# Kernel optimization log

Hardware: AMD Instinct MI355X
Metric: run time of the kernel (lower is better)

## Reference

```python
import jax, jax.numpy as jnp
import numpy as np

S, B, V, E, H = 512, 256, 100000, 128, 256


def setup_inputs() -> dict:
    key = jax.random.key(0)
    k1, k2, k3, k4, k5, k6 = jax.random.split(key, 6)
    X = jax.random.randint(k1, (S, B), 0, V)
    emb = jax.random.normal(k2, (V, E), dtype=jnp.float32)
    # PyTorch nn.RNN init: U(-1/sqrt(H), 1/sqrt(H))
    s = 1.0 / np.sqrt(H)
    W_ih = jax.random.uniform(k3, (H, E), minval=-s, maxval=s, dtype=jnp.float32)
    W_hh = jax.random.uniform(k4, (H, H), minval=-s, maxval=s, dtype=jnp.float32)
    b_ih = jax.random.uniform(k5, (H,), minval=-s, maxval=s, dtype=jnp.float32)
    b_hh = jax.random.uniform(k6, (H,), minval=-s, maxval=s, dtype=jnp.float32)
    return {"X": X, "emb": emb, "W_ih": W_ih, "W_hh": W_hh, "b_ih": b_ih, "b_hh": b_hh}


def reference(X, emb, W_ih, W_hh, b_ih, b_hh):
    embedded = emb[X]                                   # [S, B, E]
    # Precompute input projections for all timesteps (one big GEMM)
    xproj = jnp.einsum('sbe,he->sbh', embedded, W_ih) + b_ih + b_hh  # [S, B, H]
    h0 = jnp.zeros((B, H), dtype=embedded.dtype)

    def step(h, xp):
        h_new = jnp.tanh(xp + h @ W_hh.T)
        return h_new, None

    h_last, _ = jax.lax.scan(step, h0, xproj)           # [B, H]
    return jax.nn.log_softmax(h_last, axis=1)
```

## Files before the change

kernel.cpp:

```cpp
#include <hip/hip_runtime.h>
#include <math.h>

#define S_LEN 512
#define B_SZ  256
#define E_SZ  128
#define H_SZ  256
#define XSTP  65536

typedef __attribute__((ext_vector_type(8))) short bf16x8;
typedef __attribute__((ext_vector_type(4))) float f32x4;

__device__ short g_wfh[H_SZ * E_SZ];
__device__ short g_wfl[H_SZ * E_SZ];

__device__ __forceinline__ unsigned pkbf(float a, float b) {
    unsigned r; asm("v_cvt_pk_bf16_f32 %0, %1, %2" : "=v"(r) : "v"(a), "v"(b));
    return r;
}
__device__ __forceinline__ float fromlo(unsigned u) {
    union { unsigned u; float f; } c; c.u = u << 16; return c.f;
}
__device__ __forceinline__ float fromhi(unsigned u) {
    union { unsigned u; float f; } c; c.u = u & 0xffff0000u; return c.f;
}
__device__ __forceinline__ void cvt_hilo8(float4 a, float4 b, bf16x8& hi, bf16x8& lo) {
    unsigned h0 = pkbf(a.x, a.y), h1 = pkbf(a.z, a.w);
    unsigned h2 = pkbf(b.x, b.y), h3 = pkbf(b.z, b.w);
    unsigned l0 = pkbf(a.x - fromlo(h0), a.y - fromhi(h0));
    unsigned l1 = pkbf(a.z - fromlo(h1), a.w - fromhi(h1));
    unsigned l2 = pkbf(b.x - fromlo(h2), b.y - fromhi(h2));
    unsigned l3 = pkbf(b.z - fromlo(h3), b.w - fromhi(h3));
    union { bf16x8 v; unsigned u[4]; } H, L;
    H.u[0] = h0; H.u[1] = h1; H.u[2] = h2; H.u[3] = h3;
    L.u[0] = l0; L.u[1] = l1; L.u[2] = l2; L.u[3] = l3;
    hi = H.v; lo = L.v;
}

__device__ __forceinline__ float tanhC(float v) {
    float e = __builtin_amdgcn_exp2f(v * 2.8853900818f);
    return fmaf(-2.f, __builtin_amdgcn_rcpf(e + 1.f), 1.f);
}

__global__ void prep_w_kernel(const float* __restrict__ W_ih) {
    const int t  = blockIdx.x * 256 + threadIdx.x;
    const int l  = t & 63;
    const int kk = (t >> 6) & 3;
    const int ht = t >> 8;
    const int h  = ht * 16 + (l & 15);
    const int k0 = kk * 32 + (l >> 4) * 8;
    const float* wp = W_ih + h * E_SZ + k0;
    float4 a = *(const float4*)wp;
    float4 b = *(const float4*)(wp + 4);
    bf16x8 hi, lo;
    cvt_hilo8(a, b, hi, lo);
    *(bf16x8*)&g_wfh[t * 8] = hi;
    *(bf16x8*)&g_wfl[t * 8] = lo;
}

__global__ __launch_bounds__(256) void embed_proj_mfma(
    const int*   __restrict__ X,
    const float* __restrict__ emb,
    const float* __restrict__ b_ih,
    const float* __restrict__ b_hh,
    float*       __restrict__ xproj)
{
    __shared__ int   toks[32];
    __shared__ short BtH[2][4][64][8];
    __shared__ short BtL[2][4][64][8];

    const int tid  = threadIdx.x;
    const int wave = tid >> 6;
    const int lane = tid & 63;
    const int quad = lane >> 4;
    const size_t row0 = (size_t)blockIdx.x * 32;
    const int s_idx = (int)(row0 >> 8);
    const int bbase = (int)(row0 & 255);

    if (tid < 32) toks[tid] = X[row0 + tid];
    __syncthreads();

    {
        const int r  = tid >> 3;
        const int kk = (tid >> 1) & 3;
        const int hq = tid & 1;
        const float* ep = emb + (size_t)toks[r] * E_SZ + kk * 32 + hq * 16;
        float4 a0 = ((const float4*)ep)[0];
        float4 b0 = ((const float4*)ep)[1];
        float4 a1 = ((const float4*)ep)[2];
        float4 b1 = ((const float4*)ep)[3];
        bf16x8 h0, l0, h1, l1;
        cvt_hilo8(a0, b0, h0, l0);
        cvt_hilo8(a1, b1, h1, l1);
        const int q0 = hq * 2, rl = r & 15, nt = r >> 4;
        *(bf16x8*)&BtH[nt][kk][q0 * 16 + rl][0]       = h0;
        *(bf16x8*)&BtL[nt][kk][q0 * 16 + rl][0]       = l0;
        *(bf16x8*)&BtH[nt][kk][(q0 + 1) * 16 + rl][0] = h1;
        *(bf16x8*)&BtL[nt][kk][(q0 + 1) * 16 + rl][0] = l1;
    }
    __syncthreads();

#pragma unroll
    for (int mt = 0; mt < 4; ++mt) {
        const int ht = wave * 4 + mt;
        bf16x8 wh[4], wl[4];
#pragma unroll
        for (int kk = 0; kk < 4; ++kk) {
            wh[kk] = *(const bf16x8*)&g_wfh[((ht * 4 + kk) * 64 + lane) * 8];
            wl[kk] = *(const bf16x8*)&g_wfl[((ht * 4 + kk) * 64 + lane) * 8];
        }

        f32x4 acc0 = {0.f, 0.f, 0.f, 0.f};
        f32x4 acc1 = {0.f, 0.f, 0.f, 0.f};
#pragma unroll
        for (int kk = 0; kk < 4; ++kk) {
            bf16x8 bh0  = *(const bf16x8*)&BtH[0][kk][lane][0];
            bf16x8 blo0 = *(const bf16x8*)&BtL[0][kk][lane][0];
            bf16x8 bh1  = *(const bf16x8*)&BtH[1][kk][lane][0];
            bf16x8 blo1 = *(const bf16x8*)&BtL[1][kk][lane][0];
            acc0 = __builtin_amdgcn_mfma_f32_16x16x32_bf16(wh[kk], bh0,  acc0, 0, 0, 0);
            acc0 = __builtin_amdgcn_mfma_f32_16x16x32_bf16(wh[kk], blo0, acc0, 0, 0, 0);
            acc0 = __builtin_amdgcn_mfma_f32_16x16x32_bf16(wl[kk], bh0,  acc0, 0, 0, 0);
            acc1 = __builtin_amdgcn_mfma_f32_16x16x32_bf16(wh[kk], bh1,  acc1, 0, 0, 0);
            acc1 = __builtin_amdgcn_mfma_f32_16x16x32_bf16(wh[kk], blo1, acc1, 0, 0, 0);
            acc1 = __builtin_amdgcn_mfma_f32_16x16x32_bf16(wl[kk], bh1,  acc1, 0, 0, 0);
        }

        const int hb = ht * 16 + quad * 4;
        float4 bi  = *(const float4*)&b_ih[hb];
        float4 bh4 = *(const float4*)&b_hh[hb];
#pragma unroll
        for (int nt = 0; nt < 2; ++nt) {
            const int b   = bbase + nt * 16;
            const int blk = b >> 5, str = (b >> 4) & 1;
            f32x4 o = (nt == 0) ? acc0 : acc1;
            o[0] += bi.x + bh4.x; o[1] += bi.y + bh4.y;
            o[2] += bi.z + bh4.z; o[3] += bi.w + bh4.w;
            float* dst = xproj + (size_t)s_idx * XSTP
                       + ((((blk * 2 + str) * 8 + (ht >> 1)) * 2 + (ht & 1)) * 64 + lane) * 4;
            *(f32x4*)dst = o;
        }
    }
}

__global__ __launch_bounds__(512) void rnn_scan_kernel(
    const float* __restrict__ xproj,
    const float* __restrict__ W_hh,
    float*       __restrict__ out)
{
    const int tid  = threadIdx.x;
    const int wave = tid >> 6;
    const int lane = tid & 63;
    const int bl   = lane & 15;
    const int quad = lane >> 4;
    const int B0   = blockIdx.x * 16;

    __shared__ short HB[2][4096];
    __shared__ float sred[8][16];

    bf16x8 wfrag[2][8];
#pragma unroll
    for (int mt = 0; mt < 2; ++mt) {
        const int h = wave * 32 + mt * 16 + bl;
#pragma unroll
        for (int kk = 0; kk < 8; ++kk) {
            const float* wp = W_hh + (size_t)h * H_SZ + kk * 32 + quad * 8;
            float4 a = *(const float4*)wp;
            float4 b = *(const float4*)(wp + 4);
            union { bf16x8 v; unsigned u[4]; } F;
            F.u[0] = pkbf(a.x, a.y); F.u[1] = pkbf(a.z, a.w);
            F.u[2] = pkbf(b.x, b.y); F.u[3] = pkbf(b.z, b.w);
            wfrag[mt][kk] = F.v;
        }
    }

    ((int4*)&HB[0][0])[tid] = make_int4(0, 0, 0, 0);

    const int xsw = (bl & 8) << 2;

    const short* rd0 = &HB[0][0] + ((lane * 8) ^ xsw);
    const short* rd1 = &HB[1][0] + ((lane * 8) ^ xsw);

    const int wo = (wave * 512 + (quad >> 1) * 128 + bl * 8 + (quad & 1) * 4) ^ xsw;
    short* const w0 = &HB[0][0] + wo;
    short* const w1 = &HB[1][0] + wo;

    const float* xpb = xproj + ((size_t)blockIdx.x * 16 + wave * 2) * 256 + lane * 4;

    f32x4 xe0 = *(const f32x4*)(xpb);
    f32x4 xe1 = *(const f32x4*)(xpb + 256);
    f32x4 xo0 = *(const f32x4*)(xpb + XSTP);
    f32x4 xo1 = *(const f32x4*)(xpb + XSTP + 256);

    __syncthreads();

    auto do_step = [&](const short* rd, short* wr,
                       f32x4& x0, f32x4& x1, const float* pf) {
        bf16x8 bf[8];
#pragma unroll
        for (int kk = 0; kk < 8; ++kk)
            bf[kk] = *(const bf16x8*)(rd + kk * 512);

        f32x4 a0 = x0, b0 = {0.f,0.f,0.f,0.f};
#pragma unroll
        for (int kk = 0; kk < 4; ++kk) {
            a0 = __builtin_amdgcn_mfma_f32_16x16x32_bf16(wfrag[0][kk],   bf[kk],   a0, 0, 0, 0);
            b0 = __builtin_amdgcn_mfma_f32_16x16x32_bf16(wfrag[0][kk+4], bf[kk+4], b0, 0, 0, 0);
        }
        f32x4 a1 = x1, b1 = {0.f,0.f,0.f,0.f};
#pragma unroll
        for (int kk = 0; kk < 4; ++kk) {
            a1 = __builtin_amdgcn_mfma_f32_16x16x32_bf16(wfrag[1][kk],   bf[kk],   a1, 0, 0, 0);
            b1 = __builtin_amdgcn_mfma_f32_16x16x32_bf16(wfrag[1][kk+4], bf[kk+4], b1, 0, 0, 0);
        }

        const f32x4 d0 = a0 + b0;
        float t0 = tanhC(d0[0]), t1 = tanhC(d0[1]), t2 = tanhC(d0[2]), t3 = tanhC(d0[3]);
        *(uint2*)wr = make_uint2(pkbf(t0, t1), pkbf(t2, t3));

        const f32x4 d1 = a1 + b1;
        float u0 = tanhC(d1[0]), u1 = tanhC(d1[1]), u2 = tanhC(d1[2]), u3 = tanhC(d1[3]);
        *(uint2*)(wr + 256) = make_uint2(pkbf(u0, u1), pkbf(u2, u3));

        x0 = *(const f32x4*)pf;
        x1 = *(const f32x4*)(pf + 256);

        asm volatile("s_waitcnt lgkmcnt(0)" ::: "memory");
        __builtin_amdgcn_sched_barrier(0);
        __builtin_amdgcn_s_barrier();
    };

    const float* pf = xpb + 2 * (size_t)XSTP;
    for (int s = 0; s < 510; s += 2) {
        do_step(rd0, w1, xe0, xe1, pf);
        do_step(rd1, w0, xo0, xo1, pf + XSTP);
        pf += 2 * (size_t)XSTP;
    }
    do_step(rd0, w1, xe0, xe1, xpb);

    float vf0[4], vf1[4];
    {
        bf16x8 bf[8];
#pragma unroll
        for (int kk = 0; kk < 8; ++kk)
            bf[kk] = *(const bf16x8*)(rd1 + kk * 512);
        f32x4 a0 = xo0, a1 = xo1;
        f32x4 b0 = {0.f,0.f,0.f,0.f}, b1 = {0.f,0.f,0.f,0.f};
#pragma unroll
        for (int kk = 0; kk < 4; ++kk) {
            a0 = __builtin_amdgcn_mfma_f32_16x16x32_bf16(wfrag[0][kk],   bf[kk],   a0, 0, 0, 0);
            a1 = __builtin_amdgcn_mfma_f32_16x16x32_bf16(wfrag[1][kk],   bf[kk],   a1, 0, 0, 0);
            b0 = __builtin_amdgcn_mfma_f32_16x16x32_bf16(wfrag[0][kk+4], bf[kk+4], b0, 0, 0, 0);
            b1 = __builtin_amdgcn_mfma_f32_16x16x32_bf16(wfrag[1][kk+4], bf[kk+4], b1, 0, 0, 0);
        }
        const f32x4 d0 = a0 + b0, d1 = a1 + b1;
#pragma unroll
        for (int r = 0; r < 4; ++r) {
            vf0[r] = tanhC(d0[r]);
            vf1[r] = tanhC(d1[r]);
        }
    }

    float m = fmaxf(fmaxf(fmaxf(vf0[0], vf0[1]), fmaxf(vf0[2], vf0[3])),
                    fmaxf(fmaxf(vf1[0], vf1[1]), fmaxf(vf1[2], vf1[3])));
    m = fmaxf(m, __shfl_xor(m, 16));
    m = fmaxf(m, __shfl_xor(m, 32));
    if (lane < 16) sred[wave][bl] = m;
    __syncthreads();
    float mall = sred[0][bl];
#pragma unroll
    for (int w = 1; w < 8; ++w) mall = fmaxf(mall, sred[w][bl]);
    __syncthreads();

    float ss = 0.f;
#pragma unroll
    for (int r = 0; r < 4; ++r)
        ss += __expf(vf0[r] - mall) + __expf(vf1[r] - mall);
    ss += __shfl_xor(ss, 16);
    ss += __shfl_xor(ss, 32);
    if (lane < 16) sred[wave][bl] = ss;
    __syncthreads();
    float tot = sred[0][bl];
#pragma unroll
    for (int w = 1; w < 8; ++w) tot += sred[w][bl];
    const float lse = mall + __logf(tot);

    f32x4 o0, o1;
#pragma unroll
    for (int r = 0; r < 4; ++r) { o0[r] = vf0[r] - lse; o1[r] = vf1[r] - lse; }
    float* op = out + (size_t)(B0 + bl) * H_SZ + wave * 32 + quad * 4;
    *(f32x4*)op        = o0;
    *(f32x4*)(op + 16) = o1;
}

extern "C" void kernel_launch(void* const* d_in, const int* in_sizes, int n_in,
                              void* d_out, int out_size, void* d_ws, size_t ws_size,
                              hipStream_t stream) {
    const int*   X    = (const int*)  d_in[0];
    const float* emb  = (const float*)d_in[1];
    const float* W_ih = (const float*)d_in[2];
    const float* W_hh = (const float*)d_in[3];
    const float* b_ih = (const float*)d_in[4];
    const float* b_hh = (const float*)d_in[5];
    float* out   = (float*)d_out;
    float* xproj = (float*)d_ws;

    prep_w_kernel<<<dim3(16), 256, 0, stream>>>(W_ih);
    embed_proj_mfma<<<dim3((S_LEN * B_SZ) / 32), 256, 0, stream>>>(
        X, emb, b_ih, b_hh, xproj);
    rnn_scan_kernel<<<dim3(B_SZ / 16), 512, 0, stream>>>(xproj, W_hh, out);
}
```

Baseline: 408.8 us.

## Fuse embedding projection and RNN scan into one kernel with per-timestep flags

Merges the embed/projection kernel and the recurrent scan into a single launch. The first 16 blocks run the scan, and the remaining blocks produce xproj tiles and publish per-tile ready flags with release stores. Scan blocks spin on these flags before loading each timestep's projection. This lets the serial recurrence overlap with the projection GEMM instead of waiting for it to finish. The risks are correctness depending on scan blocks being scheduled first (low block IDs), the cost of atomic loads and polling, and producers competing with the scan for CU resources.

```diff
diff --git a/kernel.cpp b/kernel.cpp
--- a/kernel.cpp
+++ b/kernel.cpp
@@ -12,6 +12,7 @@
 
 __device__ short g_wfh[H_SZ * E_SZ];
 __device__ short g_wfl[H_SZ * E_SZ];
+__device__ int   g_flags[4096];
 
 __device__ __forceinline__ unsigned pkbf(float a, float b) {
     unsigned r; asm("v_cvt_pk_bf16_f32 %0, %1, %2" : "=v"(r) : "v"(a), "v"(b));
@@ -41,8 +42,21 @@
     return fmaf(-2.f, __builtin_amdgcn_rcpf(e + 1.f), 1.f);
 }
 
+__device__ __forceinline__ int flagld(const int* p) {
+    return __hip_atomic_load(p, __ATOMIC_RELAXED, __HIP_MEMORY_SCOPE_AGENT);
+}
+__device__ __forceinline__ f32x4 aload4(const float* p) {
+    f32x4 v;
+    v[0] = __hip_atomic_load(p + 0, __ATOMIC_RELAXED, __HIP_MEMORY_SCOPE_AGENT);
+    v[1] = __hip_atomic_load(p + 1, __ATOMIC_RELAXED, __HIP_MEMORY_SCOPE_AGENT);
+    v[2] = __hip_atomic_load(p + 2, __ATOMIC_RELAXED, __HIP_MEMORY_SCOPE_AGENT);
+    v[3] = __hip_atomic_load(p + 3, __ATOMIC_RELAXED, __HIP_MEMORY_SCOPE_AGENT);
+    return v;
+}
+
 __global__ void prep_w_kernel(const float* __restrict__ W_ih) {
     const int t  = blockIdx.x * 256 + threadIdx.x;
+    g_flags[t] = 0;
     const int l  = t & 63;
     const int kk = (t >> 6) & 3;
     const int ht = t >> 8;
@@ -57,105 +71,112 @@
     *(bf16x8*)&g_wfl[t * 8] = lo;
 }
 
-__global__ __launch_bounds__(256) void embed_proj_mfma(
+__global__ __launch_bounds__(512) void fused_kernel(
     const int*   __restrict__ X,
     const float* __restrict__ emb,
     const float* __restrict__ b_ih,
     const float* __restrict__ b_hh,
-    float*       __restrict__ xproj)
-{
-    __shared__ int   toks[32];
-    __shared__ short BtH[2][4][64][8];
-    __shared__ short BtL[2][4][64][8];
-
-    const int tid  = threadIdx.x;
-    const int wave = tid >> 6;
-    const int lane = tid & 63;
-    const int quad = lane >> 4;
-    const size_t row0 = (size_t)blockIdx.x * 32;
-    const int s_idx = (int)(row0 >> 8);
-    const int bbase = (int)(row0 & 255);
-
-    if (tid < 32) toks[tid] = X[row0 + tid];
-    __syncthreads();
-
-    {
-        const int r  = tid >> 3;
-        const int kk = (tid >> 1) & 3;
-        const int hq = tid & 1;
-        const float* ep = emb + (size_t)toks[r] * E_SZ + kk * 32 + hq * 16;
-        float4 a0 = ((const float4*)ep)[0];
-        float4 b0 = ((const float4*)ep)[1];
-        float4 a1 = ((const float4*)ep)[2];
-        float4 b1 = ((const float4*)ep)[3];
-        bf16x8 h0, l0, h1, l1;
-        cvt_hilo8(a0, b0, h0, l0);
-        cvt_hilo8(a1, b1, h1, l1);
-        const int q0 = hq * 2, rl = r & 15, nt = r >> 4;
-        *(bf16x8*)&BtH[nt][kk][q0 * 16 + rl][0]       = h0;
-        *(bf16x8*)&BtL[nt][kk][q0 * 16 + rl][0]       = l0;
-        *(bf16x8*)&BtH[nt][kk][(q0 + 1) * 16 + rl][0] = h1;
-        *(bf16x8*)&BtL[nt][kk][(q0 + 1) * 16 + rl][0] = l1;
-    }
-    __syncthreads();
-
-#pragma unroll
-    for (int mt = 0; mt < 4; ++mt) {
-        const int ht = wave * 4 + mt;
-        bf16x8 wh[4], wl[4];
-#pragma unroll
-        for (int kk = 0; kk < 4; ++kk) {
-            wh[kk] = *(const bf16x8*)&g_wfh[((ht * 4 + kk) * 64 + lane) * 8];
-            wl[kk] = *(const bf16x8*)&g_wfl[((ht * 4 + kk) * 64 + lane) * 8];
-        }
-
-        f32x4 acc0 = {0.f, 0.f, 0.f, 0.f};
-        f32x4 acc1 = {0.f, 0.f, 0.f, 0.f};
-#pragma unroll
-        for (int kk = 0; kk < 4; ++kk) {
-            bf16x8 bh0  = *(const bf16x8*)&BtH[0][kk][lane][0];
-            bf16x8 blo0 = *(const bf16x8*)&BtL[0][kk][lane][0];
-            bf16x8 bh1  = *(const bf16x8*)&BtH[1][kk][lane][0];
-            bf16x8 blo1 = *(const bf16x8*)&BtL[1][kk][lane][0];
-            acc0 = __builtin_amdgcn_mfma_f32_16x16x32_bf16(wh[kk], bh0,  acc0, 0, 0, 0);
-            acc0 = __builtin_amdgcn_mfma_f32_16x16x32_bf16(wh[kk], blo0, acc0, 0, 0, 0);
-            acc0 = __builtin_amdgcn_mfma_f32_16x16x32_bf16(wl[kk], bh0,  acc0, 0, 0, 0);
-            acc1 = __builtin_amdgcn_mfma_f32_16x16x32_bf16(wh[kk], bh1,  acc1, 0, 0, 0);
-            acc1 = __builtin_amdgcn_mfma_f32_16x16x32_bf16(wh[kk], blo1, acc1, 0, 0, 0);
-            acc1 = __builtin_amdgcn_mfma_f32_16x16x32_bf16(wl[kk], bh1,  acc1, 0, 0, 0);
-        }
-
-        const int hb = ht * 16 + quad * 4;
-        float4 bi  = *(const float4*)&b_ih[hb];
-        float4 bh4 = *(const float4*)&b_hh[hb];
-#pragma unroll
-        for (int nt = 0; nt < 2; ++nt) {
-            const int b   = bbase + nt * 16;
-            const int blk = b >> 5, str = (b >> 4) & 1;
-            f32x4 o = (nt == 0) ? acc0 : acc1;
-            o[0] += bi.x + bh4.x; o[1] += bi.y + bh4.y;
-            o[2] += bi.z + bh4.z; o[3] += bi.w + bh4.w;
-            float* dst = xproj + (size_t)s_idx * XSTP
-                       + ((((blk * 2 + str) * 8 + (ht >> 1)) * 2 + (ht & 1)) * 64 + lane) * 4;
-            *(f32x4*)dst = o;
-        }
-    }
-}
-
-__global__ __launch_bounds__(512) void rnn_scan_kernel(
-    const float* __restrict__ xproj,
     const float* __restrict__ W_hh,
+    float*       __restrict__ xproj,
     float*       __restrict__ out)
 {
-    const int tid  = threadIdx.x;
+    extern __shared__ char smem[];
+    const int tid = threadIdx.x;
+
+    if (blockIdx.x >= 16) {
+        const int half = tid >> 8;
+        const int tt   = tid & 255;
+        const int tl   = (int)(blockIdx.x - 16) * 2 + half;
+        char*  ebase = smem + half * 16512;
+        int*   toks  = (int*)ebase;
+        short* BtH   = (short*)(ebase + 128);
+        short* BtL   = BtH + 4096;
+
+        const int wave = tt >> 6, lane = tt & 63, quad = lane >> 4;
+        const size_t row0 = (size_t)tl * 32;
+        const int s_idx = tl >> 3;
+        const int bbase = (tl & 7) * 32;
+
+        if (tt < 32) toks[tt] = X[row0 + tt];
+        __syncthreads();
+
+        {
+            const int r = tt >> 3, kk = (tt >> 1) & 3, hq = tt & 1;
+            const float* ep = emb + (size_t)toks[r] * E_SZ + kk * 32 + hq * 16;
+            float4 a0 = ((const float4*)ep)[0];
+            float4 b0 = ((const float4*)ep)[1];
+            float4 a1 = ((const float4*)ep)[2];
+            float4 b1 = ((const float4*)ep)[3];
+            bf16x8 h0, l0, h1, l1;
+            cvt_hilo8(a0, b0, h0, l0);
+            cvt_hilo8(a1, b1, h1, l1);
+            const int q0 = hq * 2, rl = r & 15, nt = r >> 4;
+            *(bf16x8*)&BtH[((nt * 4 + kk) * 64 + q0 * 16 + rl) * 8]       = h0;
+            *(bf16x8*)&BtL[((nt * 4 + kk) * 64 + q0 * 16 + rl) * 8]       = l0;
+            *(bf16x8*)&BtH[((nt * 4 + kk) * 64 + (q0 + 1) * 16 + rl) * 8] = h1;
+            *(bf16x8*)&BtL[((nt * 4 + kk) * 64 + (q0 + 1) * 16 + rl) * 8] = l1;
+        }
+        __syncthreads();
+
+#pragma unroll
+        for (int mt = 0; mt < 4; ++mt) {
+            const int ht = wave * 4 + mt;
+            bf16x8 wh[4], wl[4];
+#pragma unroll
+            for (int kk = 0; kk < 4; ++kk) {
+                wh[kk] = *(const bf16x8*)&g_wfh[((ht * 4 + kk) * 64 + lane) * 8];
+                wl[kk] = *(const bf16x8*)&g_wfl[((ht * 4 + kk) * 64 + lane) * 8];
+            }
+            f32x4 acc0 = {0.f, 0.f, 0.f, 0.f};
+            f32x4 acc1 = {0.f, 0.f, 0.f, 0.f};
+#pragma unroll
+            for (int kk = 0; kk < 4; ++kk) {
+                bf16x8 bh0  = *(const bf16x8*)&BtH[((0 * 4 + kk) * 64 + lane) * 8];
+                bf16x8 blo0 = *(const bf16x8*)&BtL[((0 * 4 + kk) * 64 + lane) * 8];
+                bf16x8 bh1  = *(const bf16x8*)&BtH[((1 * 4 + kk) * 64 + lane) * 8];
+                bf16x8 blo1 = *(const bf16x8*)&BtL[((1 * 4 + kk) * 64 + lane) * 8];
+                acc0 = __builtin_amdgcn_mfma_f32_16x16x32_bf16(wh[kk], bh0,  acc0, 0, 0, 0);
+                acc0 = __builtin_amdgcn_mfma_f32_16x16x32_bf16(wh[kk], blo0, acc0, 0, 0, 0);
+                acc0 = __builtin_amdgcn_mfma_f32_16x16x32_bf16(wl[kk], bh0,  acc0, 0, 0, 0);
+                acc1 = __builtin_amdgcn_mfma_f32_16x16x32_bf16(wh[kk], bh1,  acc1, 0, 0, 0);
+                acc1 = __builtin_amdgcn_mfma_f32_16x16x32_bf16(wh[kk], blo1, acc1, 0, 0, 0);
+                acc1 = __builtin_amdgcn_mfma_f32_16x16x32_bf16(wl[kk], bh1,  acc1, 0, 0, 0);
+            }
+            const int hb = ht * 16 + quad * 4;
+            float4 bi  = *(const float4*)&b_ih[hb];
+            float4 bh4 = *(const float4*)&b_hh[hb];
+#pragma unroll
+            for (int nt = 0; nt < 2; ++nt) {
+                const int b   = bbase + nt * 16;
+                const int blk = b >> 5, str = (b >> 4) & 1;
+                f32x4 o = (nt == 0) ? acc0 : acc1;
+                o[0] += bi.x + bh4.x; o[1] += bi.y + bh4.y;
+                o[2] += bi.z + bh4.z; o[3] += bi.w + bh4.w;
+                float* dst = xproj + (size_t)s_idx * XSTP
+                           + ((((blk * 2 + str) * 8 + (ht >> 1)) * 2 + (ht & 1)) * 64 + lane) * 4;
+                *(f32x4*)dst = o;
+            }
+        }
+
+        __syncthreads();
+        if (tt == 0) {
+            __threadfence();
+            __hip_atomic_store(&g_flags[tl], 1, __ATOMIC_RELEASE, __HIP_MEMORY_SCOPE_AGENT);
+        }
+        return;
+    }
+
+    short* HB0 = (short*)smem;
+    short* HB1 = HB0 + 4096;
+    float* sred = (float*)(smem + 16384);
+
     const int wave = tid >> 6;
     const int lane = tid & 63;
     const int bl   = lane & 15;
     const int quad = lane >> 4;
     const int B0   = blockIdx.x * 16;
-
-    __shared__ short HB[2][4096];
-    __shared__ float sred[8][16];
+    const int j0   = blockIdx.x >> 1;
+    const int* flagbase = g_flags + j0;
 
     bf16x8 wfrag[2][8];
 #pragma unroll
@@ -173,28 +194,30 @@
         }
     }
 
-    ((int4*)&HB[0][0])[tid] = make_int4(0, 0, 0, 0);
+    ((int4*)HB0)[tid] = make_int4(0, 0, 0, 0);
 
     const int xsw = (bl & 8) << 2;
-
-    const short* rd0 = &HB[0][0] + ((lane * 8) ^ xsw);
-    const short* rd1 = &HB[1][0] + ((lane * 8) ^ xsw);
-
+    const short* rd0 = HB0 + ((lane * 8) ^ xsw);
+    const short* rd1 = HB1 + ((lane * 8) ^ xsw);
     const int wo = (wave * 512 + (quad >> 1) * 128 + bl * 8 + (quad & 1) * 4) ^ xsw;
-    short* const w0 = &HB[0][0] + wo;
-    short* const w1 = &HB[1][0] + wo;
+    short* const w0 = HB0 + wo;
+    short* const w1 = HB1 + wo;
 
     const float* xpb = xproj + ((size_t)blockIdx.x * 16 + wave * 2) * 256 + lane * 4;
 
-    f32x4 xe0 = *(const f32x4*)(xpb);
-    f32x4 xe1 = *(const f32x4*)(xpb + 256);
-    f32x4 xo0 = *(const f32x4*)(xpb + XSTP);
-    f32x4 xo1 = *(const f32x4*)(xpb + XSTP + 256);
+    while (flagld(flagbase + 0 * 8) == 0) {}
+    while (flagld(flagbase + 1 * 8) == 0) {}
+    f32x4 xe0 = aload4(xpb);
+    f32x4 xe1 = aload4(xpb + 256);
+    f32x4 xo0 = aload4(xpb + XSTP);
+    f32x4 xo1 = aload4(xpb + XSTP + 256);
+    int f_e = flagld(flagbase + 2 * 8);
+    int f_o = flagld(flagbase + 3 * 8);
 
     __syncthreads();
 
-    auto do_step = [&](const short* rd, short* wr,
-                       f32x4& x0, f32x4& x1, const float* pf) {
+    auto do_step = [&](const short* rd, short* wr, f32x4& x0, f32x4& x1,
+                       const float* pf, int& f, const int* fcur, const int* fnext) {
         bf16x8 bf[8];
 #pragma unroll
         for (int kk = 0; kk < 8; ++kk)
@@ -221,8 +244,10 @@
         float u0 = tanhC(d1[0]), u1 = tanhC(d1[1]), u2 = tanhC(d1[2]), u3 = tanhC(d1[3]);
         *(uint2*)(wr + 256) = make_uint2(pkbf(u0, u1), pkbf(u2, u3));
 
-        x0 = *(const f32x4*)pf;
-        x1 = *(const f32x4*)(pf + 256);
+        if (f == 0) { do { f = flagld(fcur); } while (f == 0); }
+        x0 = aload4(pf);
+        x1 = aload4(pf + 256);
+        f = flagld(fnext);
 
         asm volatile("s_waitcnt lgkmcnt(0)" ::: "memory");
         __builtin_amdgcn_sched_barrier(0);
@@ -231,11 +256,13 @@
 
     const float* pf = xpb + 2 * (size_t)XSTP;
     for (int s = 0; s < 510; s += 2) {
-        do_step(rd0, w1, xe0, xe1, pf);
-        do_step(rd1, w0, xo0, xo1, pf + XSTP);
+        const int ne = (s + 4 <= 511) ? (s + 4) : 511;
+        const int no = (s + 5 <= 511) ? (s + 5) : 511;
+        do_step(rd0, w1, xe0, xe1, pf,        f_e, flagbase + (s + 2) * 8, flagbase + ne * 8);
+        do_step(rd1, w0, xo0, xo1, pf + XSTP, f_o, flagbase + (s + 3) * 8, flagbase + no * 8);
         pf += 2 * (size_t)XSTP;
     }
-    do_step(rd0, w1, xe0, xe1, xpb);
+    do_step(rd0, w1, xe0, xe1, xpb, f_e, flagbase + 511 * 8, flagbase + 511 * 8);
 
     float vf0[4], vf1[4];
     {
@@ -264,11 +291,11 @@
                     fmaxf(fmaxf(vf1[0], vf1[1]), fmaxf(vf1[2], vf1[3])));
     m = fmaxf(m, __shfl_xor(m, 16));
     m = fmaxf(m, __shfl_xor(m, 32));
-    if (lane < 16) sred[wave][bl] = m;
+    if (lane < 16) sred[wave * 16 + bl] = m;
     __syncthreads();
-    float mall = sred[0][bl];
-#pragma unroll
-    for (int w = 1; w < 8; ++w) mall = fmaxf(mall, sred[w][bl]);
+    float mall = sred[0 * 16 + bl];
+#pragma unroll
+    for (int w = 1; w < 8; ++w) mall = fmaxf(mall, sred[w * 16 + bl]);
     __syncthreads();
 
     float ss = 0.f;
@@ -277,11 +304,11 @@
         ss += __expf(vf0[r] - mall) + __expf(vf1[r] - mall);
     ss += __shfl_xor(ss, 16);
     ss += __shfl_xor(ss, 32);
-    if (lane < 16) sred[wave][bl] = ss;
+    if (lane < 16) sred[wave * 16 + bl] = ss;
     __syncthreads();
-    float tot = sred[0][bl];
-#pragma unroll
-    for (int w = 1; w < 8; ++w) tot += sred[w][bl];
+    float tot = sred[0 * 16 + bl];
+#pragma unroll
+    for (int w = 1; w < 8; ++w) tot += sred[w * 16 + bl];
     const float lse = mall + __logf(tot);
 
     f32x4 o0, o1;
@@ -305,7 +332,6 @@
     float* xproj = (float*)d_ws;
 
     prep_w_kernel<<<dim3(16), 256, 0, stream>>>(W_ih);
-    embed_proj_mfma<<<dim3((S_LEN * B_SZ) / 32), 256, 0, stream>>>(
-        X, emb, b_ih, b_hh, xproj);
-    rnn_scan_kernel<<<dim3(B_SZ / 16), 512, 0, stream>>>(xproj, W_hh, out);
-}
+    fused_kernel<<<dim3(16 + 2048), 512, 33024, stream>>>(
+        X, emb, b_ih, b_hh, W_hh, xproj, out);
+}
```

Result: slower. 793.5 us (+94.1%).
